# Kernel optimization log

Hardware: AMD Instinct MI355X
Metric: run time of the kernel (lower is better)

Reference implementation:

```python
import jax, jax.numpy as jnp
import numpy as np

# Config / sizes
N = 20000       # nodes
E = 320000      # edges (avg degree 16)
IN_DIM = 6      # node feature dim
PE = 8          # laplacian PE dims
ED = 4          # edge feature dim
H = 128         # hidden dim
OUT = 4         # output dim
L = 3           # message-passing layers
T = 3           # node types (typed encoders/decoders)


def mlp(z, W1, b1, W2, b2):
    # _make_mlp: Linear -> ReLU -> Linear
    return jax.nn.relu(z @ W1 + b1) @ W2 + b2


def typed_mlp(z, W1, b1, W2, b2, types):
    # W1: [T, Din, H]; compute all T branches, select per-node by type
    h = jax.nn.relu(jnp.einsum('ni,tih->tnh', z, W1) + b1[:, None, :])
    o = jnp.einsum('tnh,tho->tno', h, W2) + b2[:, None, :]
    onehot = jax.nn.one_hot(types, W1.shape[0], dtype=o.dtype)  # [N, T]
    return jnp.einsum('tno,nt->no', o, onehot)


def setup_inputs() -> dict:
    key = jax.random.key(0)
    ks = jax.random.split(key, 40)

    def w(k, shape, fan_in):
        return jax.random.normal(k, shape, dtype=jnp.float32) / np.float32(np.sqrt(fan_in))

    inp = {}
    inp['x'] = jax.random.normal(ks[0], (N, IN_DIM), dtype=jnp.float32)
    inp['pe'] = jax.random.normal(ks[1], (N, PE), dtype=jnp.float32)
    inp['edge_attr'] = jax.random.normal(ks[2], (E, ED), dtype=jnp.float32)
    # typed node encoders: (in_dim+pe_dims) -> H -> H
    inp['enc_W1'] = w(ks[3], (T, IN_DIM + PE, H), IN_DIM + PE)
    inp['enc_b1'] = jnp.zeros((T, H), jnp.float32)
    inp['enc_W2'] = w(ks[4], (T, H, H), H)
    inp['enc_b2'] = jnp.zeros((T, H), jnp.float32)
    # edge encoder: ED -> H -> H
    inp['ee_W1'] = w(ks[5], (ED, H), ED)
    inp['ee_b1'] = jnp.zeros((H,), jnp.float32)
    inp['ee_W2'] = w(ks[6], (H, H), H)
    inp['ee_b2'] = jnp.zeros((H,), jnp.float32)
    # per-layer edge update (3H->H->H), node update (2H->H->H), fusion (H->H->H)
    inp['eu_W1'] = w(ks[7], (L, 3 * H, H), 3 * H)
    inp['eu_b1'] = jnp.zeros((L, H), jnp.float32)
    inp['eu_W2'] = w(ks[8], (L, H, H), H)
    inp['eu_b2'] = jnp.zeros((L, H), jnp.float32)
    inp['nu_W1'] = w(ks[9], (L, 2 * H, H), 2 * H)
    inp['nu_b1'] = jnp.zeros((L, H), jnp.float32)
    inp['nu_W2'] = w(ks[10], (L, H, H), H)
    inp['nu_b2'] = jnp.zeros((L, H), jnp.float32)
    inp['fu_W1'] = w(ks[11], (L, H, H), H)
    inp['fu_b1'] = jnp.zeros((L, H), jnp.float32)
    inp['fu_W2'] = w(ks[12], (L, H, H), H)
    inp['fu_b2'] = jnp.zeros((L, H), jnp.float32)
    # typed decoders: H -> H -> OUT
    inp['dec_W1'] = w(ks[13], (T, H, H), H)
    inp['dec_b1'] = jnp.zeros((T, H), jnp.float32)
    inp['dec_W2'] = w(ks[14], (T, H, OUT), H)
    inp['dec_b2'] = jnp.zeros((T, OUT), jnp.float32)
    # int inputs
    inp['edge_index'] = jax.random.randint(ks[15], (2, E), 0, N)
    inp['node_types'] = jax.random.randint(ks[16], (N,), 0, T)
    return inp


def reference(x, pe, edge_attr,
              enc_W1, enc_b1, enc_W2, enc_b2,
              ee_W1, ee_b1, ee_W2, ee_b2,
              eu_W1, eu_b1, eu_W2, eu_b2,
              nu_W1, nu_b1, nu_W2, nu_b2,
              fu_W1, fu_b1, fu_W2, fu_b2,
              dec_W1, dec_b1, dec_W2, dec_b2,
              edge_index, node_types):
    n = x.shape[0]
    src, dst = edge_index[0], edge_index[1]
    # typed node encode on [x || pe]
    h_nodes = typed_mlp(jnp.concatenate([x, pe], axis=-1),
                        enc_W1, enc_b1, enc_W2, enc_b2, node_types)
    # edge encode
    h_edges = mlp(edge_attr, ee_W1, ee_b1, ee_W2, ee_b2)
    num_layers = eu_W1.shape[0]
    for l in range(num_layers):
        # gather endpoint states, edge MLP, residual on edges
        m_edge = mlp(jnp.concatenate([h_nodes[src], h_nodes[dst], h_edges], axis=-1),
                     eu_W1[l], eu_b1[l], eu_W2[l], eu_b2[l])
        h_edges = h_edges + m_edge
        # scatter-add aggregation to destination nodes (index_add_)
        m_node = jax.ops.segment_sum(h_edges, dst, num_segments=n)
        # node update + residual, then fusion (dropout is eval/identity)
        upd = mlp(jnp.concatenate([h_nodes, m_node], axis=-1),
                  nu_W1[l], nu_b1[l], nu_W2[l], nu_b2[l])
        local = h_nodes + upd
        h_nodes = mlp(local, fu_W1[l], fu_b1[l], fu_W2[l], fu_b2[l])
    # typed decode
    out = typed_mlp(h_nodes, dec_W1, dec_b1, dec_W2, dec_b2, node_types)
    return out
```

## Files before the change

kernel.cpp:

```cpp
#include <hip/hip_runtime.h>
#include <hip/hip_bf16.h>

typedef __hip_bfloat16 bf16;
typedef __attribute__((ext_vector_type(8))) short short8;
typedef __attribute__((ext_vector_type(4))) float floatx4;

#define HDIM 128
#define NCANON 27

__device__ __forceinline__ float b2f(bf16 v) { return __bfloat162float(v); }
__device__ __forceinline__ float s2f(short s) {
  return __uint_as_float(((unsigned int)(unsigned short)s) << 16);
}
__device__ __forceinline__ short f2s(float f) {
  return (short)__bfloat16_as_ushort(__float2bfloat16(f));
}

struct CanonDesc {
  const void* src[NCANON];
  int prefix[NCANON + 1];
};

__global__ void canon_kernel(CanonDesc d, const unsigned short* __restrict__ xraw,
                             int* __restrict__ flagOut, bf16* __restrict__ out, int total,
// ... 210 lines not shown

  floatx4 acc[RT];
  #pragma unroll
  for (int rt = 0; rt < RT; rt++) acc[rt] = (floatx4){0.f, 0.f, 0.f, 0.f};
  #pragma unroll
  for (int ks = 0; ks < 4; ks++) {
    short8 bfr = *(const short8*)(W1p + (((size_t)wave * 4 + ks) * 64 + lane) * 8);
    #pragma unroll
    for (int rt = 0; rt < RT; rt++) {
      short8 a = *(const short8*)(&Zt[(rt * 16 + colq) * SK + 128 + ks * 32 + quad * 8]);
      acc[rt] = __builtin_amdgcn_mfma_f32_16x16x32_bf16(a, bfr, acc[rt], 0, 0, 0);
    }
  }
  {
    int col = wave * 16 + colq;
    float bv = b2f(b1v[col]);
    #pragma unroll
    for (int rt = 0; rt < RT; rt++)
      #pragma unroll
      for (int r = 0; r < 4; r++) {
        int lrow = rt * 16 + quad * 4 + r;
        float v = acc[rt][r] + bv + b2f(Zt[lrow * SK + col]);
        Zt[lrow * SK + col] = __float2bfloat16(fmaxf(v, 0.f));
      }
  }
  __syncthreads();

  #pragma unroll
  for (int rt = 0; rt < RT; rt++) acc[rt] = (floatx4){0.f, 0.f, 0.f, 0.f};
  #pragma unroll
  for (int ks = 0; ks < 4; ks++) {
    short8 bfr = *(const short8*)(W2p + (((size_t)wave * 4 + ks) * 64 + lane) * 8);
    #pragma unroll
    for (int rt = 0; rt < RT; rt++) {
      short8 a = *(const short8*)(&Zt[(rt * 16 + colq) * SK + ks * 32 + quad * 8]);
      acc[rt] = __builtin_amdgcn_mfma_f32_16x16x32_bf16(a, bfr, acc[rt], 0, 0, 0);
    }
  }
  {
    int col = wave * 16 + colq;
    float bv = b2f(b2v[col]);
    #pragma unroll
    for (int rt = 0; rt < RT; rt++)
      #pragma unroll
      for (int r = 0; r < 4; r++) {
        int lrow = rt * 16 + quad * 4 + r;
        float v = acc[rt][r] + bv + b2f(Zt[lrow * SK + 128 + col]);
        Zt[lrow * SK + 128 + col] = __float2bfloat16(v);
      }
  }
  __syncthreads();

  if (WRITE_HE) {
    #pragma unroll
    for (int i = tid; i < BM * 16; i += 512) {
      int row = i >> 4, seg = i & 15;
      int gr = row0 + row;
      if (gr < M)
        *(uint4*)(outp + (size_t)gr * HDIM + seg * 8) = *(const uint4*)(&Zt[row * SK + 128 + seg * 8]);
    }
  }
  {
    int col = tid & 127;
    int q4 = tid >> 7;
    int rbeg = q4 * 16, rend = rbeg + 16;
    float s = 0.f;
    int runDst = dstLds[rbeg];
    bool touchStart = true;
    for (int r = rbeg; r < rend; r++) {
      int d = dstLds[r];
      if (d != runDst) {
        if (runDst >= 0) {
          float* mp = &mnode[(size_t)runDst * HDIM + col];
          if (touchStart) atomicAdd(mp, s); else *mp = s;
        }
        runDst = d; s = 0.f; touchStart = false;
      }
      s += b2f(Zt[r * SK + 128 + col]);
    }
    if (runDst >= 0) atomicAdd(&mnode[(size_t)runDst * HDIM + col], s);
  }
}

__global__ void __launch_bounds__(512) node_kernel(
    const bf16* __restrict__ h_nodes, float* __restrict__ mnode,
    const bf16* __restrict__ nuW1, const bf16* __restrict__ nuB1,
    const bf16* __restrict__ nuW2, const bf16* __restrict__ nuB2,
    const bf16* __restrict__ fuW1, const bf16* __restrict__ fuB1,
    const bf16* __restrict__ fuW2, const bf16* __restrict__ fuB2,
    const bf16* __restrict__ yW1a, const bf16* __restrict__ yW1b,
    bf16* __restrict__ ysA, bf16* __restrict__ ysB,
    bf16* __restrict__ outp, int M) {
  constexpr int BM = 64, SK = 272;
  __shared__ bf16 Zt[BM * SK];
  const int tid = threadIdx.x;
  const int lane = tid & 63, wave = tid >> 6, colq = lane & 15, quad = lane >> 4;
  const int wr = wave >> 2, wc = wave & 3;
  const int row0 = blockIdx.x * BM;
  {
    int row = tid >> 3, sub = tid & 7;
    int gr = row0 + row;
    bool ok = gr < M;
    float4 z4 = {0.f, 0.f, 0.f, 0.f};
    #pragma unroll
    for (int j = 0; j < 4; j++) {
      int c = j * 8 + sub;
      int part = c >> 4, seg = c & 15;
      if (part == 0) {
        uint4 v = {0u, 0u, 0u, 0u};
        if (ok) v = *(const uint4*)(h_nodes + (size_t)gr * HDIM + seg * 8);
        *(uint4*)(&Zt[row * SK + seg * 8]) = v;
      } else {
        short8 o = {0, 0, 0, 0, 0, 0, 0, 0};
        if (ok) {
          float* mp = mnode + (size_t)gr * HDIM + seg * 8;
          #pragma unroll
          for (int k = 0; k < 8; k++) o[k] = f2s(mp[k]);
          if (yW1a) { *(float4*)(mp) = z4; *(float4*)(mp + 4) = z4; }
        }
        *(short8*)(&Zt[row * SK + 128 + seg * 8]) = o;
      }
    }
  }
  __syncthreads();

  floatx4 acc[2][2];
  #pragma unroll
  for (int rt = 0; rt < 2; rt++)
    #pragma unroll
    for (int c = 0; c < 2; c++) acc[rt][c] = (floatx4){0.f, 0.f, 0.f, 0.f};
  #pragma unroll
  for (int ks = 0; ks < 8; ks++) {
    short8 bfr0 = *(const short8*)(nuW1 + (((size_t)(wc * 2 + 0) * 8 + ks) * 64 + lane) * 8);
    short8 bfr1 = *(const short8*)(nuW1 + (((size_t)(wc * 2 + 1) * 8 + ks) * 64 + lane) * 8);
    #pragma unroll
    for (int rt = 0; rt < 2; rt++) {
      short8 a = *(const short8*)(&Zt[(wr * 32 + rt * 16 + colq) * SK + ks * 32 + quad * 8]);
      acc[rt][0] = __builtin_amdgcn_mfma_f32_16x16x32_bf16(a, bfr0, acc[rt][0], 0, 0, 0);
      acc[rt][1] = __builtin_amdgcn_mfma_f32_16x16x32_bf16(a, bfr1, acc[rt][1], 0, 0, 0);
    }
  }
  __syncthreads();
  #pragma unroll
  for (int c = 0; c < 2; c++) {
    int col = wc * 32 + c * 16 + colq;
    float bv = b2f(nuB1[col]);
    #pragma unroll
    for (int rt = 0; rt < 2; rt++)
      #pragma unroll
      for (int r = 0; r < 4; r++)
        Zt[(wr * 32 + rt * 16 + quad * 4 + r) * SK + 128 + col] =
            __float2bfloat16(fmaxf(acc[rt][c][r] + bv, 0.f));
  }
  __syncthreads();

  #pragma unroll
  for (int rt = 0; rt < 2; rt++)
    #pragma unroll
    for (int c = 0; c < 2; c++) acc[rt][c] = (floatx4){0.f, 0.f, 0.f, 0.f};
  #pragma unroll
  for (int ks = 0; ks < 4; ks++) {
    short8 bfr0 = *(const short8*)(nuW2 + (((size_t)(wc * 2 + 0) * 4 + ks) * 64 + lane) * 8);
    short8 bfr1 = *(const short8*)(nuW2 + (((size_t)(wc * 2 + 1) * 4 + ks) * 64 + lane) * 8);
    #pragma unroll
    for (int rt = 0; rt < 2; rt++) {
      short8 a = *(const short8*)(&Zt[(wr * 32 + rt * 16 + colq) * SK + 128 + ks * 32 + quad * 8]);
// ... 40 lines not shown
      #pragma unroll
      for (int r = 0; r < 4; r++)
        Zt[(wr * 32 + rt * 16 + quad * 4 + r) * SK + 128 + col] =
            __float2bfloat16(fmaxf(acc[rt][c][r] + bv, 0.f));
  }
  __syncthreads();

  #pragma unroll
  for (int rt = 0; rt < 2; rt++)
    #pragma unroll
    for (int c = 0; c < 2; c++) acc[rt][c] = (floatx4){0.f, 0.f, 0.f, 0.f};
  #pragma unroll
  for (int ks = 0; ks < 4; ks++) {
    short8 bfr0 = *(const short8*)(fuW2 + (((size_t)(wc * 2 + 0) * 4 + ks) * 64 + lane) * 8);
    short8 bfr1 = *(const short8*)(fuW2 + (((size_t)(wc * 2 + 1) * 4 + ks) * 64 + lane) * 8);
    #pragma unroll
    for (int rt = 0; rt < 2; rt++) {
      short8 a = *(const short8*)(&Zt[(wr * 32 + rt * 16 + colq) * SK + 128 + ks * 32 + quad * 8]);
      acc[rt][0] = __builtin_amdgcn_mfma_f32_16x16x32_bf16(a, bfr0, acc[rt][0], 0, 0, 0);
      acc[rt][1] = __builtin_amdgcn_mfma_f32_16x16x32_bf16(a, bfr1, acc[rt][1], 0, 0, 0);
    }
  }
  #pragma unroll
  for (int c = 0; c < 2; c++) {
    int col = wc * 32 + c * 16 + colq;
    float bv = b2f(fuB2[col]);
    #pragma unroll
    for (int rt = 0; rt < 2; rt++)
      #pragma unroll
      for (int r = 0; r < 4; r++) {
        int lrow = wr * 32 + rt * 16 + quad * 4 + r;
        Zt[lrow * SK + col] = __float2bfloat16(acc[rt][c][r] + bv);
      }
  }
  __syncthreads();
  for (int i = tid; i < BM * 16; i += 512) {
    int row = i >> 4, seg = i & 15;
    int gr = row0 + row;
    if (gr < M)
      *(uint4*)(outp + (size_t)gr * HDIM + seg * 8) = *(const uint4*)(&Zt[row * SK + seg * 8]);
  }
  if (!yW1a) return;

  #pragma unroll
  for (int which = 0; which < 2; which++) {
    const bf16* Wp = which ? yW1b : yW1a;
    bf16* outy = which ? ysB : ysA;
    #pragma unroll
    for (int rt = 0; rt < 2; rt++)
      #pragma unroll
      for (int c = 0; c < 2; c++) acc[rt][c] = (floatx4){0.f, 0.f, 0.f, 0.f};
    #pragma unroll
    for (int ks = 0; ks < 4; ks++) {
      short8 bfr0 = *(const short8*)(Wp + (((size_t)(wc * 2 + 0) * 4 + ks) * 64 + lane) * 8);
      short8 bfr1 = *(const short8*)(Wp + (((size_t)(wc * 2 + 1) * 4 + ks) * 64 + lane) * 8);
      #pragma unroll
      for (int rt = 0; rt < 2; rt++) {
        short8 a = *(const short8*)(&Zt[(wr * 32 + rt * 16 + colq) * SK + ks * 32 + quad * 8]);
        acc[rt][0] = __builtin_amdgcn_mfma_f32_16x16x32_bf16(a, bfr0, acc[rt][0], 0, 0, 0);
        acc[rt][1] = __builtin_amdgcn_mfma_f32_16x16x32_bf16(a, bfr1, acc[rt][1], 0, 0, 0);
      }
    }
    #pragma unroll
    for (int c = 0; c < 2; c++) {
      int col = wc * 32 + c * 16 + colq;
      #pragma unroll
      for (int rt = 0; rt < 2; rt++)
        #pragma unroll
        for (int r = 0; r < 4; r++)
          Zt[(wr * 32 + rt * 16 + quad * 4 + r) * SK + 128 + col] =
              __float2bfloat16(acc[rt][c][r]);
    }
    __syncthreads();
    for (int i = tid; i < BM * 16; i += 512) {
      int row = i >> 4, seg = i & 15;
      int gr = row0 + row;
      if (gr < M)
        *(uint4*)(outy + (size_t)gr * HDIM + seg * 8) = *(const uint4*)(&Zt[row * SK + 128 + seg * 8]);
    }
    __syncthreads();
  }
}

__global__ void __launch_bounds__(512) encee_kernel(
    int eeBlocks, int ngrid64,
    const bf16* __restrict__ eaS,
    const bf16* __restrict__ eeW1, const bf16* __restrict__ eeB1,
    const bf16* __restrict__ eeW2, const bf16* __restrict__ eeB2,
    bf16* __restrict__ h_edges, int E,
    const bf16* __restrict__ x, const bf16* __restrict__ pe,
    const int* __restrict__ perm, const int* __restrict__ ts,
    const bf16* __restrict__ encW1, const bf16* __restrict__ encB1,
    const bf16* __restrict__ encW2, const bf16* __restrict__ encB2,
    bf16* __restrict__ h_nodes,
    const bf16* __restrict__ yW1a, const bf16* __restrict__ yW1b,
    bf16* __restrict__ ysA, bf16* __restrict__ ysB) {
  __shared__ bf16 smem[128 * 144];
  __shared__ int gIdx[64];
  const int tid = threadIdx.x;
  const int lane = tid & 63, wave = tid >> 6, colq = lane & 15, quad = lane >> 4;
  const int wr = wave >> 2, wc = wave & 3;

  if (blockIdx.x < eeBlocks) {
    constexpr int BM = 128, RT = 4, SK = 144;
    bf16* Zt = smem;
    const int row0 = blockIdx.x * BM;
    {
      int i = tid;
      int row = i >> 2, seg = i & 3;
      int gr = row0 + row;
      uint4 val = {0u, 0u, 0u, 0u};
      if (seg == 0 && gr < E) {
        uint2 v = *(const uint2*)(eaS + (size_t)gr * 4);
        val.x = v.x; val.y = v.y;
      }
      *(uint4*)(&Zt[row * SK + seg * 8]) = val;
    }
    __syncthreads();
    floatx4 acc[RT][2];
    #pragma unroll
    for (int rt = 0; rt < RT; rt++)
      #pragma unroll
      for (int c = 0; c < 2; c++) acc[rt][c] = (floatx4){0.f, 0.f, 0.f, 0.f};
    {
      short8 bfr0 = *(const short8*)(eeW1 + (((size_t)(wc * 2 + 0)) * 64 + lane) * 8);
      short8 bfr1 = *(const short8*)(eeW1 + (((size_t)(wc * 2 + 1)) * 64 + lane) * 8);
      #pragma unroll
      for (int rt = 0; rt < RT; rt++) {
        short8 a = *(const short8*)(&Zt[(wr * 64 + rt * 16 + colq) * SK + quad * 8]);
        acc[rt][0] = __builtin_amdgcn_mfma_f32_16x16x32_bf16(a, bfr0, acc[rt][0], 0, 0, 0);
        acc[rt][1] = __builtin_amdgcn_mfma_f32_16x16x32_bf16(a, bfr1, acc[rt][1], 0, 0, 0);
      }
    }
    __syncthreads();
    #pragma unroll
    for (int c = 0; c < 2; c++) {
      int col = wc * 32 + c * 16 + colq;
      float bv = b2f(eeB1[col]);
      #pragma unroll
      for (int rt = 0; rt < RT; rt++)
        #pragma unroll
        for (int r = 0; r < 4; r++)
          Zt[(wr * 64 + rt * 16 + quad * 4 + r) * SK + col] =
              __float2bfloat16(fmaxf(acc[rt][c][r] + bv, 0.f));
    }
    __syncthreads();
    floatx4 acc2[RT][2];
    #pragma unroll
    for (int rt = 0; rt < RT; rt++)
      #pragma unroll
      for (int c = 0; c < 2; c++) acc2[rt][c] = (floatx4){0.f, 0.f, 0.f, 0.f};
    #pragma unroll
    for (int ks = 0; ks < 4; ks++) {
      short8 bfr0 = *(const short8*)(eeW2 + (((size_t)(wc * 2 + 0) * 4 + ks) * 64 + lane) * 8);
      short8 bfr1 = *(const short8*)(eeW2 + (((size_t)(wc * 2 + 1) * 4 + ks) * 64 + lane) * 8);
      #pragma unroll
      for (int rt = 0; rt < RT; rt++) {
        short8 a = *(const short8*)(&Zt[(wr * 64 + rt * 16 + colq) * SK + ks * 32 + quad * 8]);
        acc2[rt][0] = __builtin_amdgcn_mfma_f32_16x16x32_bf16(a, bfr0, acc2[rt][0], 0, 0, 0);
        acc2[rt][1] = __builtin_amdgcn_mfma_f32_16x16x32_bf16(a, bfr1, acc2[rt][1], 0, 0, 0);
      }
    }
    __syncthreads();
    #pragma unroll
    for (int c = 0; c < 2; c++) {
      int col = wc * 32 + c * 16 + colq;
      float bv = b2f(eeB2[col]);
      #pragma unroll
      for (int rt = 0; rt < RT; rt++)
        #pragma unroll
        for (int r = 0; r < 4; r++)
          Zt[(wr * 64 + rt * 16 + quad * 4 + r) * SK + col] =
              __float2bfloat16(acc2[rt][c][r] + bv);
    }
    __syncthreads();
    for (int i = tid; i < BM * 16; i += 512) {
      int row = i >> 4, seg = i & 15;
      int gr = row0 + row;
      if (gr < E)
        *(uint4*)(h_edges + (size_t)gr * HDIM + seg * 8) = *(const uint4*)(&Zt[row * SK + seg * 8]);
    }
    return;
  }

  {
    constexpr int BM = 64, SKz = 40, HS = 144;
    bf16* Zt = smem;
    bf16* Hid = smem + BM * SKz;
    int idx = blockIdx.x - eeBlocks;
    int t = idx / ngrid64;
    int bx = idx - t * ngrid64;
    int rs = ts[t], re = ts[t + 1];
    int row0 = rs + bx * BM;
    if (row0 >= re) return;
    for (int i = tid; i < BM; i += 512) gIdx[i] = (row0 + i < re) ? perm[row0 + i] : -1;
    __syncthreads();
    for (int i = tid; i < BM * 32; i += 512) {
      int row = i >> 5, k = i & 31;
      int g = gIdx[row];
      bf16 v = __float2bfloat16(0.f);
      if (g >= 0 && k < 14) v = (k < 6) ? x[(size_t)g * 6 + k] : pe[(size_t)g * 8 + (k - 6)];
      Zt[row * SKz + k] = v;
    }
    __syncthreads();
    const bf16* W1t = encW1 + (size_t)t * 4096;
    const bf16* W2t = encW2 + (size_t)t * 16384;
    floatx4 acc[2][2];
    #pragma unroll
    for (int rt = 0; rt < 2; rt++)
      #pragma unroll
      for (int c = 0; c < 2; c++) acc[rt][c] = (floatx4){0.f, 0.f, 0.f, 0.f};
    {
      short8 bfr0 = *(const short8*)(W1t + (((size_t)(wc * 2 + 0)) * 64 + lane) * 8);
      short8 bfr1 = *(const short8*)(W1t + (((size_t)(wc * 2 + 1)) * 64 + lane) * 8);
      #pragma unroll
      for (int rt = 0; rt < 2; rt++) {
        short8 a = *(const short8*)(&Zt[(wr * 32 + rt * 16 + colq) * SKz + quad * 8]);
        acc[rt][0] = __builtin_amdgcn_mfma_f32_16x16x32_bf16(a, bfr0, acc[rt][0], 0, 0, 0);
        acc[rt][1] = __builtin_amdgcn_mfma_f32_16x16x32_bf16(a, bfr1, acc[rt][1], 0, 0, 0);
      }
    }
    #pragma unroll
    for (int c = 0; c < 2; c++) {
      int col = wc * 32 + c * 16 + colq;
      float bv = b2f(encB1[t * HDIM + col]);
      #pragma unroll
      for (int rt = 0; rt < 2; rt++)
        #pragma unroll
        for (int r = 0; r < 4; r++)
          Hid[(wr * 32 + rt * 16 + quad * 4 + r) * HS + col] =
              __float2bfloat16(fmaxf(acc[rt][c][r] + bv, 0.f));
    }
    __syncthreads();
    floatx4 acc2[2][2];
    #pragma unroll
    for (int rt = 0; rt < 2; rt++)
      #pragma unroll
      for (int c = 0; c < 2; c++) acc2[rt][c] = (floatx4){0.f, 0.f, 0.f, 0.f};
    #pragma unroll
    for (int ks = 0; ks < 4; ks++) {
      short8 bfr0 = *(const short8*)(W2t + (((size_t)(wc * 2 + 0) * 4 + ks) * 64 + lane) * 8);
      short8 bfr1 = *(const short8*)(W2t + (((size_t)(wc * 2 + 1) * 4 + ks) * 64 + lane) * 8);
      #pragma unroll
      for (int rt = 0; rt < 2; rt++) {
        short8 a = *(const short8*)(&Hid[(wr * 32 + rt * 16 + colq) * HS + ks * 32 + quad * 8]);
        acc2[rt][0] = __builtin_amdgcn_mfma_f32_16x16x32_bf16(a, bfr0, acc2[rt][0], 0, 0, 0);
        acc2[rt][1] = __builtin_amdgcn_mfma_f32_16x16x32_bf16(a, bfr1, acc2[rt][1], 0, 0, 0);
      }
    }
    __syncthreads();
    #pragma unroll
    for (int c = 0; c < 2; c++) {
      int col = wc * 32 + c * 16 + colq;
      float bv = b2f(encB2[t * HDIM + col]);
      #pragma unroll
      for (int rt = 0; rt < 2; rt++)
        #pragma unroll
        for (int r = 0; r < 4; r++) {
          int row = wr * 32 + rt * 16 + quad * 4 + r;
          int g = gIdx[row];
          bf16 hb = __float2bfloat16(acc2[rt][c][r] + bv);
          Hid[row * HS + col] = hb;
          if (g >= 0) h_nodes[(size_t)g * HDIM + col] = hb;
        }
    }
    __syncthreads();

    #pragma unroll
    for (int which = 0; which < 2; which++) {
      const bf16* Wp = which ? yW1b : yW1a;
      bf16* outy = which ? ysB : ysA;
      floatx4 accy[2][2];
      #pragma unroll
      for (int rt = 0; rt < 2; rt++)
        #pragma unroll
        for (int c = 0; c < 2; c++) accy[rt][c] = (floatx4){0.f, 0.f, 0.f, 0.f};
      #pragma unroll
      for (int ks = 0; ks < 4; ks++) {
        short8 bfr0 = *(const short8*)(Wp + (((size_t)(wc * 2 + 0) * 4 + ks) * 64 + lane) * 8);
        short8 bfr1 = *(const short8*)(Wp + (((size_t)(wc * 2 + 1) * 4 + ks) * 64 + lane) * 8);
        #pragma unroll
        for (int rt = 0; rt < 2; rt++) {
          short8 a = *(const short8*)(&Hid[(wr * 32 + rt * 16 + colq) * HS + ks * 32 + quad * 8]);
          accy[rt][0] = __builtin_amdgcn_mfma_f32_16x16x32_bf16(a, bfr0, accy[rt][0], 0, 0, 0);
          accy[rt][1] = __builtin_amdgcn_mfma_f32_16x16x32_bf16(a, bfr1, accy[rt][1], 0, 0, 0);
        }
      }
      #pragma unroll
      for (int c = 0; c < 2; c++) {
        int col = wc * 32 + c * 16 + colq;
        #pragma unroll
        for (int rt = 0; rt < 2; rt++)
          #pragma unroll
          for (int r = 0; r < 4; r++) {
            int g = gIdx[wr * 32 + rt * 16 + quad * 4 + r];
            if (g >= 0) outy[(size_t)g * HDIM + col] = __float2bfloat16(accy[rt][c][r]);
          }
      }
    }
  }
}

__global__ void __launch_bounds__(256) dec_kernel(
    const bf16* __restrict__ in0,
    const int* __restrict__ perm, const int* __restrict__ ts, const int* __restrict__ flagp,
    const bf16* __restrict__ W1p, const bf16* __restrict__ b1v,
    const bf16* __restrict__ W2p, const bf16* __restrict__ b2v,
    void* __restrict__ outp) {
  constexpr int BM = 64, RT = 4, SK = 144, HS = 144;
  int t = blockIdx.y;
  int rs = ts[t], re = ts[t + 1];
  int row0 = rs + blockIdx.x * BM;
  if (row0 >= re) return;
  __shared__ bf16 Zt[BM * SK];
  __shared__ bf16 Hid[BM * HS];
  __shared__ int gIdx[BM];
  const int tid = threadIdx.x;
  const int lane = tid & 63, wave = tid >> 6, colq = lane & 15, quad = lane >> 4;
  for (int i = tid; i < BM; i += 256) gIdx[i] = (row0 + i < re) ? perm[row0 + i] : -1;
  __syncthreads();
  {
    int row = tid >> 2, sub = tid & 3;
    int g = gIdx[row];
    #pragma unroll
    for (int j = 0; j < 4; j++) {
      int seg = j * 4 + sub;
      uint4 v = {0u, 0u, 0u, 0u};
      if (g >= 0) v = *(const uint4*)(in0 + (size_t)g * HDIM + seg * 8);
      *(uint4*)(&Zt[row * SK + seg * 8]) = v;
    }
  }
  __syncthreads();
  const bf16* W1t = W1p + (size_t)t * 16384;
  const bf16* W2t = W2p + (size_t)t * 16384;
  floatx4 acc[RT][2];
  #pragma unroll
  for (int rt = 0; rt < RT; rt++)
    #pragma unroll
    for (int c = 0; c < 2; c++) acc[rt][c] = (floatx4){0.f, 0.f, 0.f, 0.f};
  #pragma unroll
  for (int ks = 0; ks < 4; ks++) {
    short8 bfr0 = *(const short8*)(W1t + (((size_t)(wave * 2 + 0) * 4 + ks) * 64 + lane) * 8);
    short8 bfr1 = *(const short8*)(W1t + (((size_t)(wave * 2 + 1) * 4 + ks) * 64 + lane) * 8);
    #pragma unroll
    for (int rt = 0; rt < RT; rt++) {
      short8 a = *(const short8*)(&Zt[(rt * 16 + colq) * SK + ks * 32 + quad * 8]);
      acc[rt][0] = __builtin_amdgcn_mfma_f32_16x16x32_bf16(a, bfr0, acc[rt][0], 0, 0, 0);
      acc[rt][1] = __builtin_amdgcn_mfma_f32_16x16x32_bf16(a, bfr1, acc[rt][1], 0, 0, 0);
    }
  }
  #pragma unroll
  for (int c = 0; c < 2; c++) {
    int col = wave * 32 + c * 16 + colq;
    float bv = b2f(b1v[t * HDIM + col]);
    #pragma unroll
    for (int rt = 0; rt < RT; rt++)
      #pragma unroll
      for (int r = 0; r < 4; r++)
        Hid[(rt * 16 + quad * 4 + r) * HS + col] =
            __float2bfloat16(fmaxf(acc[rt][c][r] + bv, 0.f));
  }
  __syncthreads();
  floatx4 acc2[RT];
  #pragma unroll
  for (int rt = 0; rt < RT; rt++) acc2[rt] = (floatx4){0.f, 0.f, 0.f, 0.f};
  #pragma unroll
  for (int ks = 0; ks < 4; ks++) {
    short8 bfr0 = *(const short8*)(W2t + (((size_t)0 * 4 + ks) * 64 + lane) * 8);
    #pragma unroll
    for (int rt = 0; rt < RT; rt++) {
      short8 a = *(const short8*)(&Hid[(rt * 16 + colq) * HS + ks * 32 + quad * 8]);
      acc2[rt] = __builtin_amdgcn_mfma_f32_16x16x32_bf16(a, bfr0, acc2[rt], 0, 0, 0);
    }
  }
  if (wave == 0 && colq < 4) {
    int isBf = flagp[0];
    float bv = b2f(b2v[t * 4 + colq]);
    #pragma unroll
    for (int rt = 0; rt < RT; rt++)
      #pragma unroll
      for (int r = 0; r < 4; r++) {
// ... 53 lines not shown
  bf16* decW1p = (bf16*)alloc(3 * 16384 * 2);
  bf16* decW2p = (bf16*)alloc(3 * 16384 * 2);
  bf16* euW1a  = (bf16*)alloc((size_t)L * 16384 * 2);
  bf16* euW1b  = (bf16*)alloc((size_t)L * 16384 * 2);
  bf16* euW1c  = (bf16*)alloc((size_t)L * 16384 * 2);
  bf16* euW2p  = (bf16*)alloc((size_t)L * 16384 * 2);
  bf16* nuW1p  = (bf16*)alloc((size_t)L * 32768 * 2);
  bf16* nuW2p  = (bf16*)alloc((size_t)L * 16384 * 2);
  bf16* fuW1p  = (bf16*)alloc((size_t)L * 16384 * 2);
  bf16* fuW2p  = (bf16*)alloc((size_t)L * 16384 * 2);

  const bf16* cX     = arena + cd.prefix[0];
  const bf16* cPE    = arena + cd.prefix[1];
  const bf16* cEA    = arena + cd.prefix[2];
  const bf16* cEncW1 = arena + cd.prefix[3];
  const bf16* cEncB1 = arena + cd.prefix[4];
  const bf16* cEncW2 = arena + cd.prefix[5];
  const bf16* cEncB2 = arena + cd.prefix[6];
  const bf16* cEeW1  = arena + cd.prefix[7];
  const bf16* cEeB1  = arena + cd.prefix[8];
  const bf16* cEeW2  = arena + cd.prefix[9];
  const bf16* cEeB2  = arena + cd.prefix[10];
  const bf16* cEuW1  = arena + cd.prefix[11];
  const bf16* cEuB1  = arena + cd.prefix[12];
  const bf16* cEuW2  = arena + cd.prefix[13];
  const bf16* cEuB2  = arena + cd.prefix[14];
  const bf16* cNuW1  = arena + cd.prefix[15];
  const bf16* cNuB1  = arena + cd.prefix[16];
  const bf16* cNuW2  = arena + cd.prefix[17];
  const bf16* cNuB2  = arena + cd.prefix[18];
  const bf16* cFuW1  = arena + cd.prefix[19];
  const bf16* cFuB1  = arena + cd.prefix[20];
  const bf16* cFuW2  = arena + cd.prefix[21];
  const bf16* cFuB2  = arena + cd.prefix[22];
  const bf16* cDecW1 = arena + cd.prefix[23];
  const bf16* cDecB1 = arena + cd.prefix[24];
  const bf16* cDecW2 = arena + cd.prefix[25];
  const bf16* cDecB2 = arena + cd.prefix[26];

  int canonBlocks = (total + 255) / 256;
  size_t zbytes = (size_t)((char*)cursor - (char*)m_node) + (size_t)N * 4;
  int zquads = (int)(zbytes / 16);
  int zBlocks = (zquads + 255) / 256;
  canon_kernel<<<canonBlocks + zBlocks, 256, 0, stream>>>(
      cd, (const unsigned short*)d_in[0], flag, arena, total, canonBlocks,
      (uint4*)m_node, zquads);

  int hb = (E + 1023) / 1024;
  hist_tsort_kernel<<<hb + 1, 1024, 0, stream>>>(dstI, counts, E, hb,
                                                 node_types, tsArr, permT, N);

  PackJobs PJ;
  int nj = 0;
  PJ.j[nj++] = {cEeW1, eeW1p, 4, 1, 128};
  PJ.j[nj++] = {cEeW2, eeW2p, 128, 4, 128};
  for (int l = 0; l < L; l++) {
    const bf16* w1 = cEuW1 + (size_t)l * 384 * HDIM;
    PJ.j[nj++] = {w1,                 euW1a + (size_t)l * 16384, 128, 4, 128};
    PJ.j[nj++] = {w1 + 128 * HDIM,    euW1b + (size_t)l * 16384, 128, 4, 128};
    PJ.j[nj++] = {w1 + 256 * HDIM,    euW1c + (size_t)l * 16384, 128, 4, 128};
    PJ.j[nj++] = {cEuW2 + (size_t)l * HDIM * HDIM, euW2p + (size_t)l * 16384, 128, 4, 128};
    PJ.j[nj++] = {cNuW1 + (size_t)l * 256 * HDIM,  nuW1p + (size_t)l * 32768, 256, 8, 128};
    PJ.j[nj++] = {cNuW2 + (size_t)l * HDIM * HDIM, nuW2p + (size_t)l * 16384, 128, 4, 128};
    PJ.j[nj++] = {cFuW1 + (size_t)l * HDIM * HDIM, fuW1p + (size_t)l * 16384, 128, 4, 128};
    PJ.j[nj++] = {cFuW2 + (size_t)l * HDIM * HDIM, fuW2p + (size_t)l * 16384, 128, 4, 128};
  }
  for (int t = 0; t < 3; t++) {
    PJ.j[nj++] = {cEncW1 + (size_t)t * 14 * HDIM,   encW1p + (size_t)t * 4096, 14, 1, 128};
    PJ.j[nj++] = {cEncW2 + (size_t)t * HDIM * HDIM, encW2p + (size_t)t * 16384, 128, 4, 128};
    PJ.j[nj++] = {cDecW1 + (size_t)t * HDIM * HDIM, decW1p + (size_t)t * 16384, 128, 4, 128};
    PJ.j[nj++] = {cDecW2 + (size_t)t * HDIM * 4,    decW2p + (size_t)t * 16384, 128, 4, 4};
  }
  pack_all_kernel<<<dim3(16, nj), 256, 0, stream>>>(PJ);

  int nb = (N + 255) / 256;
  scan1_kernel<<<nb, 256, 0, stream>>>(counts, bsum, N);
  scan2_kernel<<<1, 64, 0, stream>>>(bsum, nb);
  scan3_kernel<<<nb, 256, 0, stream>>>(counts, bsum, row_start, N, nb);
  scatter_kernel<<<(E + 255) / 256, 256, 0, stream>>>(srcI, dstI, row_start, cursor,
                                                      cEA, eaS, srcS, dstS, E);

  int ngrid64  = (N + 63) / 64;
  int egrid64  = (E + 63) / 64;
  int egrid128 = (E + 127) / 128;

  encee_kernel<<<egrid128 + 3 * ngrid64, 512, 0, stream>>>(
      egrid128, ngrid64,
      eaS, eeW1p, cEeB1, eeW2p, cEeB2, h_edges, E,
      cX, cPE, permT, tsArr, encW1p, cEncB1, encW2p, cEncB2, h_nodes,
      euW1a, euW1b, ysrcb, ydstb);

  for (int l = 0; l < L; l++) {
    if (l + 1 < L) {
      eu_kernel<true><<<egrid64, 512, 0, stream>>>(
          h_edges, ysrcb, ydstb, srcS, dstS,
          euW1c + (size_t)l * 16384, cEuB1 + l * HDIM,
          euW2p + (size_t)l * 16384, cEuB2 + l * HDIM, h_edges, m_node, E);
    } else {
      eu_kernel<false><<<egrid64, 512, 0, stream>>>(
          h_edges, ysrcb, ydstb, srcS, dstS,
          euW1c + (size_t)l * 16384, cEuB1 + l * HDIM,
          euW2p + (size_t)l * 16384, cEuB2 + l * HDIM, h_edges, m_node, E);
    }
    bool hasNext = (l + 1 < L);
    node_kernel<<<ngrid64, 512, 0, stream>>>(
        h_nodes, m_node,
        nuW1p + (size_t)l * 32768, cNuB1 + l * HDIM,
        nuW2p + (size_t)l * 16384, cNuB2 + l * HDIM,
        fuW1p + (size_t)l * 16384, cFuB1 + l * HDIM,
        fuW2p + (size_t)l * 16384, cFuB2 + l * HDIM,
        hasNext ? euW1a + (size_t)(l + 1) * 16384 : nullptr,
        hasNext ? euW1b + (size_t)(l + 1) * 16384 : nullptr,
        ysrcb, ydstb, h_nodes, N);
  }

  dec_kernel<<<dim3(ngrid64, 3), 256, 0, stream>>>(
      h_nodes, permT, tsArr, flag, decW1p, cDecB1, decW2p, cDecB2, d_out);
  (void)n_in; (void)ws_size;
}
```

Before: 452.1 us.

## Fuse edge encoder into first-layer edge update kernel

The edge-encoder MLP is moved out of the combined encoder kernel and fused into a new kernel that also runs the layer-0 edge update and scatter-add. The encoded edge features stay in shared memory instead of being written to and re-read from global memory, which removes one full pass over the edge tensor. The node encoder now runs as its own kernel, serialized before the fused edge kernel, so node and edge encoding no longer overlap in one launch. The fused kernel also remaps block indices across XCDs.

```diff
diff --git a/kernel.cpp b/kernel.cpp
--- a/kernel.cpp
+++ b/kernel.cpp
@@ -316,6 +316,182 @@
   }
 }
 
+__global__ void __launch_bounds__(512) eeeu_kernel(
+    const bf16* __restrict__ eaS,
+    const bf16* __restrict__ eeW1, const bf16* __restrict__ eeB1,
+    const bf16* __restrict__ eeW2, const bf16* __restrict__ eeB2,
+    const bf16* __restrict__ ysrc, const bf16* __restrict__ ydst,
+    const int* __restrict__ srcS, const int* __restrict__ dstS,
+    const bf16* __restrict__ W1p, const bf16* __restrict__ b1v,
+    const bf16* __restrict__ W2p, const bf16* __restrict__ b2v,
+    bf16* __restrict__ outp, float* __restrict__ mnode, int M) {
+  constexpr int BM = 64, RT = 4, SK = 272;
+  __shared__ bf16 Zt[BM * SK];
+  __shared__ int dstLds[BM];
+  const int tid = threadIdx.x;
+  const int lane = tid & 63, wave = tid >> 6, colq = lane & 15, quad = lane >> 4;
+  const int nwg = gridDim.x, bid = blockIdx.x;
+  const int qq = nwg >> 3, rr = nwg & 7;
+  const int xcd = bid & 7, bidx = bid >> 3;
+  const int blk = (xcd < rr ? xcd * (qq + 1) : rr * (qq + 1) + (xcd - rr) * qq) + bidx;
+  const int row0 = blk * BM;
+  {
+    int row = tid >> 3, sub = tid & 7;
+    int gr = row0 + row;
+    bool ok = gr < M;
+    int g0 = ok ? srcS[gr] : 0;
+    int g1 = ok ? dstS[gr] : 0;
+    if (sub == 0) dstLds[row] = ok ? g1 : -1;
+    #pragma unroll
+    for (int j = 0; j < 2; j++) {
+      int seg = j * 8 + sub;
+      short8 o = {0, 0, 0, 0, 0, 0, 0, 0};
+      if (ok) {
+        short8 a = *(const short8*)(ysrc + (size_t)g0 * HDIM + seg * 8);
+        short8 b = *(const short8*)(ydst + (size_t)g1 * HDIM + seg * 8);
+        #pragma unroll
+        for (int k = 0; k < 8; k++) o[k] = f2s(s2f(a[k]) + s2f(b[k]));
+      }
+      *(short8*)(&Zt[row * SK + seg * 8]) = o;
+    }
+    if (sub < 4) {
+      uint4 v = {0u, 0u, 0u, 0u};
+      if (sub == 0 && ok) {
+        uint2 e2 = *(const uint2*)(eaS + (size_t)gr * 4);
+        v.x = e2.x; v.y = e2.y;
+      }
+      *(uint4*)(&Zt[row * SK + 128 + sub * 8]) = v;
+    }
+  }
+  __syncthreads();
+
+  floatx4 acc[RT];
+  #pragma unroll
+  for (int rt = 0; rt < RT; rt++) acc[rt] = (floatx4){0.f, 0.f, 0.f, 0.f};
+  {
+    short8 bfr = *(const short8*)(eeW1 + ((size_t)wave * 64 + lane) * 8);
+    #pragma unroll
+    for (int rt = 0; rt < RT; rt++) {
+      short8 a = *(const short8*)(&Zt[(rt * 16 + colq) * SK + 128 + quad * 8]);
+      acc[rt] = __builtin_amdgcn_mfma_f32_16x16x32_bf16(a, bfr, acc[rt], 0, 0, 0);
+    }
+  }
+  __syncthreads();
+  {
+    int col = wave * 16 + colq;
+    float bv = b2f(eeB1[col]);
+    #pragma unroll
+    for (int rt = 0; rt < RT; rt++)
+      #pragma unroll
+      for (int r = 0; r < 4; r++)
+        Zt[(rt * 16 + quad * 4 + r) * SK + 128 + col] =
+            __float2bfloat16(fmaxf(acc[rt][r] + bv, 0.f));
+  }
+  __syncthreads();
+
+  #pragma unroll
+  for (int rt = 0; rt < RT; rt++) acc[rt] = (floatx4){0.f, 0.f, 0.f, 0.f};
+  #pragma unroll
+  for (int ks = 0; ks < 4; ks++) {
+    short8 bfr = *(const short8*)(eeW2 + (((size_t)wave * 4 + ks) * 64 + lane) * 8);
+    #pragma unroll
+    for (int rt = 0; rt < RT; rt++) {
+      short8 a = *(const short8*)(&Zt[(rt * 16 + colq) * SK + 128 + ks * 32 + quad * 8]);
+      acc[rt] = __builtin_amdgcn_mfma_f32_16x16x32_bf16(a, bfr, acc[rt], 0, 0, 0);
+    }
+  }
+  __syncthreads();
+  {
+    int col = wave * 16 + colq;
+    float bv = b2f(eeB2[col]);
+    #pragma unroll
+    for (int rt = 0; rt < RT; rt++)
+      #pragma unroll
+      for (int r = 0; r < 4; r++)
+        Zt[(rt * 16 + quad * 4 + r) * SK + 128 + col] =
+            __float2bfloat16(acc[rt][r] + bv);
+  }
+  __syncthreads();
+
+  #pragma unroll
+  for (int rt = 0; rt < RT; rt++) acc[rt] = (floatx4){0.f, 0.f, 0.f, 0.f};
+  #pragma unroll
+  for (int ks = 0; ks < 4; ks++) {
+    short8 bfr = *(const short8*)(W1p + (((size_t)wave * 4 + ks) * 64 + lane) * 8);
+    #pragma unroll
+    for (int rt = 0; rt < RT; rt++) {
+      short8 a = *(const short8*)(&Zt[(rt * 16 + colq) * SK + 128 + ks * 32 + quad * 8]);
+      acc[rt] = __builtin_amdgcn_mfma_f32_16x16x32_bf16(a, bfr, acc[rt], 0, 0, 0);
+    }
+  }
+  {
+    int col = wave * 16 + colq;
+    float bv = b2f(b1v[col]);
+    #pragma unroll
+    for (int rt = 0; rt < RT; rt++)
+      #pragma unroll
+      for (int r = 0; r < 4; r++) {
+        int lrow = rt * 16 + quad * 4 + r;
+        float v = acc[rt][r] + bv + b2f(Zt[lrow * SK + col]);
+        Zt[lrow * SK + col] = __float2bfloat16(fmaxf(v, 0.f));
+      }
+  }
+  __syncthreads();
+
+  #pragma unroll
+  for (int rt = 0; rt < RT; rt++) acc[rt] = (floatx4){0.f, 0.f, 0.f, 0.f};
+  #pragma unroll
+  for (int ks = 0; ks < 4; ks++) {
+    short8 bfr = *(const short8*)(W2p + (((size_t)wave * 4 + ks) * 64 + lane) * 8);
+    #pragma unroll
+    for (int rt = 0; rt < RT; rt++) {
+      short8 a = *(const short8*)(&Zt[(rt * 16 + colq) * SK + ks * 32 + quad * 8]);
+      acc[rt] = __builtin_amdgcn_mfma_f32_16x16x32_bf16(a, bfr, acc[rt], 0, 0, 0);
+    }
+  }
+  {
+    int col = wave * 16 + colq;
+    float bv = b2f(b2v[col]);
+    #pragma unroll
+    for (int rt = 0; rt < RT; rt++)
+      #pragma unroll
+      for (int r = 0; r < 4; r++) {
+        int lrow = rt * 16 + quad * 4 + r;
+        float v = acc[rt][r] + bv + b2f(Zt[lrow * SK + 128 + col]);
+        Zt[lrow * SK + 128 + col] = __float2bfloat16(v);
+      }
+  }
+  __syncthreads();
+
+  #pragma unroll
+  for (int i = tid; i < BM * 16; i += 512) {
+    int row = i >> 4, seg = i & 15;
+    int gr = row0 + row;
+    if (gr < M)
+      *(uint4*)(outp + (size_t)gr * HDIM + seg * 8) = *(const uint4*)(&Zt[row * SK + 128 + seg * 8]);
+  }
+  {
+    int col = tid & 127;
+    int q4 = tid >> 7;
+    int rbeg = q4 * 16, rend = rbeg + 16;
+    float s = 0.f;
+    int runDst = dstLds[rbeg];
+    bool touchStart = true;
+    for (int r = rbeg; r < rend; r++) {
+      int d = dstLds[r];
+      if (d != runDst) {
+        if (runDst >= 0) {
+          float* mp = &mnode[(size_t)runDst * HDIM + col];
+          if (touchStart) atomicAdd(mp, s); else *mp = s;
+        }
+        runDst = d; s = 0.f; touchStart = false;
+      }
+      s += b2f(Zt[r * SK + 128 + col]);
+    }
+    if (runDst >= 0) atomicAdd(&mnode[(size_t)runDst * HDIM + col], s);
+  }
+}
+
 __global__ void __launch_bounds__(512) node_kernel(
     const bf16* __restrict__ h_nodes, float* __restrict__ mnode,
     const bf16* __restrict__ nuW1, const bf16* __restrict__ nuB1,
@@ -522,12 +698,8 @@
   }
 }
 
-__global__ void __launch_bounds__(512) encee_kernel(
-    int eeBlocks, int ngrid64,
-    const bf16* __restrict__ eaS,
-    const bf16* __restrict__ eeW1, const bf16* __restrict__ eeB1,
-    const bf16* __restrict__ eeW2, const bf16* __restrict__ eeB2,
-    bf16* __restrict__ h_edges, int E,
+__global__ void __launch_bounds__(512) enc_kernel(
+    int ngrid64,
     const bf16* __restrict__ x, const bf16* __restrict__ pe,
     const int* __restrict__ perm, const int* __restrict__ ts,
     const bf16* __restrict__ encW1, const bf16* __restrict__ encB1,
@@ -535,208 +707,121 @@
     bf16* __restrict__ h_nodes,
     const bf16* __restrict__ yW1a, const bf16* __restrict__ yW1b,
     bf16* __restrict__ ysA, bf16* __restrict__ ysB) {
-  __shared__ bf16 smem[128 * 144];
-  __shared__ int gIdx[64];
+  constexpr int BM = 64, SKz = 40, HS = 144;
+  __shared__ bf16 Zt[BM * SKz];
+  __shared__ bf16 Hid[BM * HS];
+  __shared__ int gIdx[BM];
   const int tid = threadIdx.x;
   const int lane = tid & 63, wave = tid >> 6, colq = lane & 15, quad = lane >> 4;
   const int wr = wave >> 2, wc = wave & 3;
-
-  if (blockIdx.x < eeBlocks) {
-    constexpr int BM = 128, RT = 4, SK = 144;
-    bf16* Zt = smem;
-    const int row0 = blockIdx.x * BM;
-    {
-      int i = tid;
-      int row = i >> 2, seg = i & 3;
-      int gr = row0 + row;
-      uint4 val = {0u, 0u, 0u, 0u};
-      if (seg == 0 && gr < E) {
-        uint2 v = *(const uint2*)(eaS + (size_t)gr * 4);
-        val.x = v.x; val.y = v.y;
-      }
-      *(uint4*)(&Zt[row * SK + seg * 8]) = val;
-    }
-    __syncthreads();
-    floatx4 acc[RT][2];
-    #pragma unroll
-    for (int rt = 0; rt < RT; rt++)
-      #pragma unroll
-      for (int c = 0; c < 2; c++) acc[rt][c] = (floatx4){0.f, 0.f, 0.f, 0.f};
-    {
-      short8 bfr0 = *(const short8*)(eeW1 + (((size_t)(wc * 2 + 0)) * 64 + lane) * 8);
-      short8 bfr1 = *(const short8*)(eeW1 + (((size_t)(wc * 2 + 1)) * 64 + lane) * 8);
-      #pragma unroll
-      for (int rt = 0; rt < RT; rt++) {
-        short8 a = *(const short8*)(&Zt[(wr * 64 + rt * 16 + colq) * SK + quad * 8]);
-        acc[rt][0] = __builtin_amdgcn_mfma_f32_16x16x32_bf16(a, bfr0, acc[rt][0], 0, 0, 0);
-        acc[rt][1] = __builtin_amdgcn_mfma_f32_16x16x32_bf16(a, bfr1, acc[rt][1], 0, 0, 0);
-      }
-    }
-    __syncthreads();
+  int t = blockIdx.x / ngrid64;
+  int bx = blockIdx.x - t * ngrid64;
+  int rs = ts[t], re = ts[t + 1];
+  int row0 = rs + bx * BM;
+  if (row0 >= re) return;
+  for (int i = tid; i < BM; i += 512) gIdx[i] = (row0 + i < re) ? perm[row0 + i] : -1;
+  __syncthreads();
+  for (int i = tid; i < BM * 32; i += 512) {
+    int row = i >> 5, k = i & 31;
+    int g = gIdx[row];
+    bf16 v = __float2bfloat16(0.f);
+    if (g >= 0 && k < 14) v = (k < 6) ? x[(size_t)g * 6 + k] : pe[(size_t)g * 8 + (k - 6)];
+    Zt[row * SKz + k] = v;
+  }
+  __syncthreads();
+  const bf16* W1t = encW1 + (size_t)t * 4096;
+  const bf16* W2t = encW2 + (size_t)t * 16384;
+  floatx4 acc[2][2];
+  #pragma unroll
+  for (int rt = 0; rt < 2; rt++)
+    #pragma unroll
+    for (int c = 0; c < 2; c++) acc[rt][c] = (floatx4){0.f, 0.f, 0.f, 0.f};
+  {
+    short8 bfr0 = *(const short8*)(W1t + (((size_t)(wc * 2 + 0)) * 64 + lane) * 8);
+    short8 bfr1 = *(const short8*)(W1t + (((size_t)(wc * 2 + 1)) * 64 + lane) * 8);
+    #pragma unroll
+    for (int rt = 0; rt < 2; rt++) {
+      short8 a = *(const short8*)(&Zt[(wr * 32 + rt * 16 + colq) * SKz + quad * 8]);
+      acc[rt][0] = __builtin_amdgcn_mfma_f32_16x16x32_bf16(a, bfr0, acc[rt][0], 0, 0, 0);
+      acc[rt][1] = __builtin_amdgcn_mfma_f32_16x16x32_bf16(a, bfr1, acc[rt][1], 0, 0, 0);
+    }
+  }
+  #pragma unroll
+  for (int c = 0; c < 2; c++) {
+    int col = wc * 32 + c * 16 + colq;
+    float bv = b2f(encB1[t * HDIM + col]);
+    #pragma unroll
+    for (int rt = 0; rt < 2; rt++)
+      #pragma unroll
+      for (int r = 0; r < 4; r++)
+        Hid[(wr * 32 + rt * 16 + quad * 4 + r) * HS + col] =
+            __float2bfloat16(fmaxf(acc[rt][c][r] + bv, 0.f));
+  }
+  __syncthreads();
+  floatx4 acc2[2][2];
+  #pragma unroll
+  for (int rt = 0; rt < 2; rt++)
+    #pragma unroll
+    for (int c = 0; c < 2; c++) acc2[rt][c] = (floatx4){0.f, 0.f, 0.f, 0.f};
+  #pragma unroll
+  for (int ks = 0; ks < 4; ks++) {
+    short8 bfr0 = *(const short8*)(W2t + (((size_t)(wc * 2 + 0) * 4 + ks) * 64 + lane) * 8);
+    short8 bfr1 = *(const short8*)(W2t + (((size_t)(wc * 2 + 1) * 4 + ks) * 64 + lane) * 8);
+    #pragma unroll
+    for (int rt = 0; rt < 2; rt++) {
+      short8 a = *(const short8*)(&Hid[(wr * 32 + rt * 16 + colq) * HS + ks * 32 + quad * 8]);
+      acc2[rt][0] = __builtin_amdgcn_mfma_f32_16x16x32_bf16(a, bfr0, acc2[rt][0], 0, 0, 0);
+      acc2[rt][1] = __builtin_amdgcn_mfma_f32_16x16x32_bf16(a, bfr1, acc2[rt][1], 0, 0, 0);
+    }
+  }
+  __syncthreads();
+  #pragma unroll
+  for (int c = 0; c < 2; c++) {
+    int col = wc * 32 + c * 16 + colq;
+    float bv = b2f(encB2[t * HDIM + col]);
+    #pragma unroll
+    for (int rt = 0; rt < 2; rt++)
+      #pragma unroll
+      for (int r = 0; r < 4; r++) {
+        int row = wr * 32 + rt * 16 + quad * 4 + r;
+        int g = gIdx[row];
+        bf16 hb = __float2bfloat16(acc2[rt][c][r] + bv);
+        Hid[row * HS + col] = hb;
+        if (g >= 0) h_nodes[(size_t)g * HDIM + col] = hb;
+      }
+  }
+  __syncthreads();
+
+  #pragma unroll
+  for (int which = 0; which < 2; which++) {
+    const bf16* Wp = which ? yW1b : yW1a;
+    bf16* outy = which ? ysB : ysA;
+    floatx4 accy[2][2];
+    #pragma unroll
+    for (int rt = 0; rt < 2; rt++)
+      #pragma unroll
+      for (int c = 0; c < 2; c++) accy[rt][c] = (floatx4){0.f, 0.f, 0.f, 0.f};
+    #pragma unroll
+    for (int ks = 0; ks < 4; ks++) {
+      short8 bfr0 = *(const short8*)(Wp + (((size_t)(wc * 2 + 0) * 4 + ks) * 64 + lane) * 8);
+      short8 bfr1 = *(const short8*)(Wp + (((size_t)(wc * 2 + 1) * 4 + ks) * 64 + lane) * 8);
+      #pragma unroll
+      for (int rt = 0; rt < 2; rt++) {
+        short8 a = *(const short8*)(&Hid[(wr * 32 + rt * 16 + colq) * HS + ks * 32 + quad * 8]);
+        accy[rt][0] = __builtin_amdgcn_mfma_f32_16x16x32_bf16(a, bfr0, accy[rt][0], 0, 0, 0);
+        accy[rt][1] = __builtin_amdgcn_mfma_f32_16x16x32_bf16(a, bfr1, accy[rt][1], 0, 0, 0);
+      }
+    }
     #pragma unroll
     for (int c = 0; c < 2; c++) {
       int col = wc * 32 + c * 16 + colq;
-      float bv = b2f(eeB1[col]);
-      #pragma unroll
-      for (int rt = 0; rt < RT; rt++)
-        #pragma unroll
-        for (int r = 0; r < 4; r++)
-          Zt[(wr * 64 + rt * 16 + quad * 4 + r) * SK + col] =
-              __float2bfloat16(fmaxf(acc[rt][c][r] + bv, 0.f));
-    }
-    __syncthreads();
-    floatx4 acc2[RT][2];
-    #pragma unroll
-    for (int rt = 0; rt < RT; rt++)
-      #pragma unroll
-      for (int c = 0; c < 2; c++) acc2[rt][c] = (floatx4){0.f, 0.f, 0.f, 0.f};
-    #pragma unroll
-    for (int ks = 0; ks < 4; ks++) {
-      short8 bfr0 = *(const short8*)(eeW2 + (((size_t)(wc * 2 + 0) * 4 + ks) * 64 + lane) * 8);
-      short8 bfr1 = *(const short8*)(eeW2 + (((size_t)(wc * 2 + 1) * 4 + ks) * 64 + lane) * 8);
-      #pragma unroll
-      for (int rt = 0; rt < RT; rt++) {
-        short8 a = *(const short8*)(&Zt[(wr * 64 + rt * 16 + colq) * SK + ks * 32 + quad * 8]);
-        acc2[rt][0] = __builtin_amdgcn_mfma_f32_16x16x32_bf16(a, bfr0, acc2[rt][0], 0, 0, 0);
-        acc2[rt][1] = __builtin_amdgcn_mfma_f32_16x16x32_bf16(a, bfr1, acc2[rt][1], 0, 0, 0);
-      }
-    }
-    __syncthreads();
-    #pragma unroll
-    for (int c = 0; c < 2; c++) {
-      int col = wc * 32 + c * 16 + colq;
-      float bv = b2f(eeB2[col]);
-      #pragma unroll
-      for (int rt = 0; rt < RT; rt++)
-        #pragma unroll
-        for (int r = 0; r < 4; r++)
-          Zt[(wr * 64 + rt * 16 + quad * 4 + r) * SK + col] =
-              __float2bfloat16(acc2[rt][c][r] + bv);
-    }
-    __syncthreads();
-    for (int i = tid; i < BM * 16; i += 512) {
-      int row = i >> 4, seg = i & 15;
-      int gr = row0 + row;
-      if (gr < E)
-        *(uint4*)(h_edges + (size_t)gr * HDIM + seg * 8) = *(const uint4*)(&Zt[row * SK + seg * 8]);
-    }
-    return;
-  }
-
-  {
-    constexpr int BM = 64, SKz = 40, HS = 144;
-    bf16* Zt = smem;
-    bf16* Hid = smem + BM * SKz;
-    int idx = blockIdx.x - eeBlocks;
-    int t = idx / ngrid64;
-    int bx = idx - t * ngrid64;
-    int rs = ts[t], re = ts[t + 1];
-    int row0 = rs + bx * BM;
-    if (row0 >= re) return;
-    for (int i = tid; i < BM; i += 512) gIdx[i] = (row0 + i < re) ? perm[row0 + i] : -1;
-    __syncthreads();
-    for (int i = tid; i < BM * 32; i += 512) {
-      int row = i >> 5, k = i & 31;
-      int g = gIdx[row];
-      bf16 v = __float2bfloat16(0.f);
-      if (g >= 0 && k < 14) v = (k < 6) ? x[(size_t)g * 6 + k] : pe[(size_t)g * 8 + (k - 6)];
-      Zt[row * SKz + k] = v;
-    }
-    __syncthreads();
-    const bf16* W1t = encW1 + (size_t)t * 4096;
-    const bf16* W2t = encW2 + (size_t)t * 16384;
-    floatx4 acc[2][2];
-    #pragma unroll
-    for (int rt = 0; rt < 2; rt++)
-      #pragma unroll
-      for (int c = 0; c < 2; c++) acc[rt][c] = (floatx4){0.f, 0.f, 0.f, 0.f};
-    {
-      short8 bfr0 = *(const short8*)(W1t + (((size_t)(wc * 2 + 0)) * 64 + lane) * 8);
-      short8 bfr1 = *(const short8*)(W1t + (((size_t)(wc * 2 + 1)) * 64 + lane) * 8);
-      #pragma unroll
-      for (int rt = 0; rt < 2; rt++) {
-        short8 a = *(const short8*)(&Zt[(wr * 32 + rt * 16 + colq) * SKz + quad * 8]);
-        acc[rt][0] = __builtin_amdgcn_mfma_f32_16x16x32_bf16(a, bfr0, acc[rt][0], 0, 0, 0);
-        acc[rt][1] = __builtin_amdgcn_mfma_f32_16x16x32_bf16(a, bfr1, acc[rt][1], 0, 0, 0);
-      }
-    }
-    #pragma unroll
-    for (int c = 0; c < 2; c++) {
-      int col = wc * 32 + c * 16 + colq;
-      float bv = b2f(encB1[t * HDIM + col]);
-      #pragma unroll
-      for (int rt = 0; rt < 2; rt++)
-        #pragma unroll
-        for (int r = 0; r < 4; r++)
-          Hid[(wr * 32 + rt * 16 + quad * 4 + r) * HS + col] =
-              __float2bfloat16(fmaxf(acc[rt][c][r] + bv, 0.f));
-    }
-    __syncthreads();
-    floatx4 acc2[2][2];
-    #pragma unroll
-    for (int rt = 0; rt < 2; rt++)
-      #pragma unroll
-      for (int c = 0; c < 2; c++) acc2[rt][c] = (floatx4){0.f, 0.f, 0.f, 0.f};
-    #pragma unroll
-    for (int ks = 0; ks < 4; ks++) {
-      short8 bfr0 = *(const short8*)(W2t + (((size_t)(wc * 2 + 0) * 4 + ks) * 64 + lane) * 8);
-      short8 bfr1 = *(const short8*)(W2t + (((size_t)(wc * 2 + 1) * 4 + ks) * 64 + lane) * 8);
-      #pragma unroll
-      for (int rt = 0; rt < 2; rt++) {
-        short8 a = *(const short8*)(&Hid[(wr * 32 + rt * 16 + colq) * HS + ks * 32 + quad * 8]);
-        acc2[rt][0] = __builtin_amdgcn_mfma_f32_16x16x32_bf16(a, bfr0, acc2[rt][0], 0, 0, 0);
-        acc2[rt][1] = __builtin_amdgcn_mfma_f32_16x16x32_bf16(a, bfr1, acc2[rt][1], 0, 0, 0);
-      }
-    }
-    __syncthreads();
-    #pragma unroll
-    for (int c = 0; c < 2; c++) {
-      int col = wc * 32 + c * 16 + colq;
-      float bv = b2f(encB2[t * HDIM + col]);
       #pragma unroll
       for (int rt = 0; rt < 2; rt++)
         #pragma unroll
         for (int r = 0; r < 4; r++) {
-          int row = wr * 32 + rt * 16 + quad * 4 + r;
-          int g = gIdx[row];
-          bf16 hb = __float2bfloat16(acc2[rt][c][r] + bv);
-          Hid[row * HS + col] = hb;
-          if (g >= 0) h_nodes[(size_t)g * HDIM + col] = hb;
+          int g = gIdx[wr * 32 + rt * 16 + quad * 4 + r];
+          if (g >= 0) outy[(size_t)g * HDIM + col] = __float2bfloat16(accy[rt][c][r]);
         }
-    }
-    __syncthreads();
-
-    #pragma unroll
-    for (int which = 0; which < 2; which++) {
-      const bf16* Wp = which ? yW1b : yW1a;
-      bf16* outy = which ? ysB : ysA;
-      floatx4 accy[2][2];
-      #pragma unroll
-      for (int rt = 0; rt < 2; rt++)
-        #pragma unroll
-        for (int c = 0; c < 2; c++) accy[rt][c] = (floatx4){0.f, 0.f, 0.f, 0.f};
-      #pragma unroll
-      for (int ks = 0; ks < 4; ks++) {
-        short8 bfr0 = *(const short8*)(Wp + (((size_t)(wc * 2 + 0) * 4 + ks) * 64 + lane) * 8);
-        short8 bfr1 = *(const short8*)(Wp + (((size_t)(wc * 2 + 1) * 4 + ks) * 64 + lane) * 8);
-        #pragma unroll
-        for (int rt = 0; rt < 2; rt++) {
-          short8 a = *(const short8*)(&Hid[(wr * 32 + rt * 16 + colq) * HS + ks * 32 + quad * 8]);
-          accy[rt][0] = __builtin_amdgcn_mfma_f32_16x16x32_bf16(a, bfr0, accy[rt][0], 0, 0, 0);
-          accy[rt][1] = __builtin_amdgcn_mfma_f32_16x16x32_bf16(a, bfr1, accy[rt][1], 0, 0, 0);
-        }
-      }
-      #pragma unroll
-      for (int c = 0; c < 2; c++) {
-        int col = wc * 32 + c * 16 + colq;
-        #pragma unroll
-        for (int rt = 0; rt < 2; rt++)
-          #pragma unroll
-          for (int r = 0; r < 4; r++) {
-            int g = gIdx[wr * 32 + rt * 16 + quad * 4 + r];
-            if (g >= 0) outy[(size_t)g * HDIM + col] = __float2bfloat16(accy[rt][c][r]);
-          }
-      }
     }
   }
 }
@@ -956,25 +1041,29 @@
 
   int ngrid64  = (N + 63) / 64;
   int egrid64  = (E + 63) / 64;
-  int egrid128 = (E + 127) / 128;
-
-  encee_kernel<<<egrid128 + 3 * ngrid64, 512, 0, stream>>>(
-      egrid128, ngrid64,
-      eaS, eeW1p, cEeB1, eeW2p, cEeB2, h_edges, E,
-      cX, cPE, permT, tsArr, encW1p, cEncB1, encW2p, cEncB2, h_nodes,
+
+  enc_kernel<<<3 * ngrid64, 512, 0, stream>>>(
+      ngrid64, cX, cPE, permT, tsArr, encW1p, cEncB1, encW2p, cEncB2, h_nodes,
       euW1a, euW1b, ysrcb, ydstb);
 
+  eeeu_kernel<<<egrid64, 512, 0, stream>>>(
+      eaS, eeW1p, cEeB1, eeW2p, cEeB2,
+      ysrcb, ydstb, srcS, dstS,
+      euW1c, cEuB1, euW2p, cEuB2, h_edges, m_node, E);
+
   for (int l = 0; l < L; l++) {
-    if (l + 1 < L) {
-      eu_kernel<true><<<egrid64, 512, 0, stream>>>(
-          h_edges, ysrcb, ydstb, srcS, dstS,
-          euW1c + (size_t)l * 16384, cEuB1 + l * HDIM,
-          euW2p + (size_t)l * 16384, cEuB2 + l * HDIM, h_edges, m_node, E);
-    } else {
-      eu_kernel<false><<<egrid64, 512, 0, stream>>>(
-          h_edges, ysrcb, ydstb, srcS, dstS,
-          euW1c + (size_t)l * 16384, cEuB1 + l * HDIM,
-          euW2p + (size_t)l * 16384, cEuB2 + l * HDIM, h_edges, m_node, E);
+    if (l > 0) {
+      if (l + 1 < L) {
+        eu_kernel<true><<<egrid64, 512, 0, stream>>>(
+            h_edges, ysrcb, ydstb, srcS, dstS,
+            euW1c + (size_t)l * 16384, cEuB1 + l * HDIM,
+            euW2p + (size_t)l * 16384, cEuB2 + l * HDIM, h_edges, m_node, E);
+      } else {
+        eu_kernel<false><<<egrid64, 512, 0, stream>>>(
+            h_edges, ysrcb, ydstb, srcS, dstS,
+            euW1c + (size_t)l * 16384, cEuB1 + l * HDIM,
+            euW2p + (size_t)l * 16384, cEuB2 + l * HDIM, h_edges, m_node, E);
+      }
     }
     bool hasNext = (l + 1 < L);
     node_kernel<<<ngrid64, 512, 0, stream>>>(
```

Result: faster. 439.8 us, median of 2 (-2.7%).
